# Optimization experiments

Measured on AMD Instinct MI355X. Metric: run time of the kernel, lower is better.

Reference implementation:

```python
import jax, jax.numpy as jnp
import numpy as np

NB_HEAD = 16
SIZE_PER_HEAD = 64
D_MODEL = NB_HEAD * SIZE_PER_HEAD  # 1024
B, S = 4, 2048
NEG_BIG = 1e10


def setup_inputs() -> dict:
    key = jax.random.key(0)
    ks = jax.random.split(key, 9)
    glorot = lambda k, shape: jax.random.uniform(
        k, shape, jnp.float32, -1.0, 1.0) * np.sqrt(6.0 / (shape[0] + shape[1]))
    return {
        "Q_emb": jax.random.normal(ks[0], (B, S, D_MODEL), jnp.float32),
        "K_emb": jax.random.normal(ks[1], (B, S, D_MODEL), jnp.float32),
        "V_emb": jax.random.normal(ks[2], (B, S, D_MODEL), jnp.float32),
        "Q_ini": jax.random.randint(ks[3], (B, S), 0, 50),
        "K_ini": jax.random.randint(ks[4], (B, S), 0, 50),
        "WQ": glorot(ks[5], (D_MODEL, D_MODEL)),
        "WK": glorot(ks[6], (D_MODEL, D_MODEL)),
        "WV": glorot(ks[7], (D_MODEL, D_MODEL)),
        "WO": glorot(ks[8], (D_MODEL, D_MODEL)),
    }


def _proj(x, W):
    # [B,S,D] @ [D, H*dh] -> [B,H,S,dh]
    b, s, _ = x.shape
    y = jnp.einsum('bsd,de->bse', x, W)
    return y.reshape(b, s, NB_HEAD, SIZE_PER_HEAD).transpose(0, 2, 1, 3)


def reference(Q_emb, K_emb, V_emb, Q_ini, K_ini, WQ, WK, WV, WO):
    b, sq, _ = Q_emb.shape
    sk = K_emb.shape[1]
    q = _proj(Q_emb, WQ)
    k = _proj(K_emb, WK)
    v = _proj(V_emb, WV)
    scores = jnp.einsum('bhqd,bhkd->bhqk', q, k) / jnp.sqrt(
        jnp.asarray(SIZE_PER_HEAD, scores_dtype := q.dtype))
    # pad mask: 1 where key token id != 0, broadcast over queries
    pad = (K_ini != 0).astype(scores.dtype)[:, None, None, :]  # [B,1,1,Sk]
    # sub mask: cumsum of eye along rows == lower-triangular causal mask
    causal = jnp.tril(jnp.ones((sq, sk), scores.dtype))[None, None]  # [1,1,Sq,Sk]
    mask = jnp.minimum(pad, causal)
    scores = scores - (1.0 - mask) * NEG_BIG
    attn = jax.nn.softmax(scores, axis=-1)
    ctx = jnp.einsum('bhqk,bhkd->bhqd', attn, v)
    ctx = ctx.transpose(0, 2, 1, 3).reshape(b, sq, NB_HEAD * SIZE_PER_HEAD)
    return jnp.einsum('bsd,de->bse', ctx, WO)
```

## Files before the change

### kernel.cpp

```cpp
#include <hip/hip_runtime.h>

typedef __bf16 bf16_t;
typedef __bf16 bf16x8 __attribute__((ext_vector_type(8)));
typedef float  f32x4  __attribute__((ext_vector_type(4)));

#define S_LEN 2048
#define NH    16
#define DH    64
#define DM    1024
#define BATCH 4

static __device__ __forceinline__ f32x4 mfma16(bf16x8 a, bf16x8 b, f32x4 c) {
    return __builtin_amdgcn_mfma_f32_16x16x32_bf16(a, b, c, 0, 0, 0);
}

static __device__ __forceinline__ void gl_lds16(const bf16_t* g, bf16_t* l) {
    __builtin_amdgcn_global_load_lds(
        (const __attribute__((address_space(1))) unsigned int*)g,
        (__attribute__((address_space(3))) unsigned int*)l, 16, 0, 0);
}

__global__ __launch_bounds__(256) void cvt_bf16(const float* __restrict__ s,
                                                bf16_t* __restrict__ d, int n) {
    int i = (blockIdx.x * 256 + threadIdx.x) * 8;
    if (i >= n) return;
    const float4* q = (const float4*)(s + i);
    float4 a = q[0], b = q[1];
    bf16x8 r;
    r[0] = (bf16_t)a.x; r[1] = (bf16_t)a.y; r[2] = (bf16_t)a.z; r[3] = (bf16_t)a.w;
    r[4] = (bf16_t)b.x; r[5] = (bf16_t)b.y; r[6] = (bf16_t)b.z; r[7] = (bf16_t)b.w;
    *(bf16x8*)(d + i) = r;
}

__global__ __launch_bounds__(256) void wtrans(const float* __restrict__ W,
                                              bf16_t* __restrict__ Wt, float scale) {
    __shared__ bf16_t tile[32][33];
    int x = threadIdx.x, ty = threadIdx.y;
    int bx = blockIdx.x * 32, by = blockIdx.y * 32;
#pragma unroll
    for (int i = 0; i < 4; ++i) {
        int y = ty * 4 + i;
        tile[y][x] = (bf16_t)(W[(by + y) * DM + bx + x] * scale);
    }
    __syncthreads();
#pragma unroll
    for (int i = 0; i < 4; ++i) {
        int y = ty * 4 + i;
        Wt[(bx + y) * DM + by + x] = tile[x][y];
    }
}

__global__ __launch_bounds__(256) void btrans(const bf16_t* __restrict__ src,
                                              bf16_t* __restrict__ dst,
                                              int R, int C) {
    __shared__ bf16_t tile[32][33];
    int x = threadIdx.x, ty = threadIdx.y;
    int bx = blockIdx.x * 32, by = blockIdx.y * 32;
#pragma unroll
    for (int i = 0; i < 4; ++i) {
        int y = ty * 4 + i;
        tile[y][x] = src[(size_t)(by + y) * C + bx + x];
    }
    __syncthreads();
#pragma unroll
    for (int i = 0; i < 4; ++i) {
        int y = ty * 4 + i;
        dst[(size_t)(bx + y) * R + by + x] = tile[x][y];
    }
}

template <typename CT>
__global__ __launch_bounds__(256) void gemm_nt_128(const bf16_t* __restrict__ A,
                                                   const bf16_t* __restrict__ Bt,
                                                   CT* __restrict__ C,
                                                   int M, int N, int K, float alpha) {
    __shared__ __align__(16) bf16_t As[128 * 32];
    __shared__ __align__(16) bf16_t Bs[128 * 32];
    int tid = threadIdx.x, wave = tid >> 6, lane = tid & 63;
    int l15 = lane & 15, quad = lane >> 4;
    int wm = wave >> 1, wn = wave & 1;
    int bm = blockIdx.x * 128, bn = blockIdx.y * 128;
    int lrow = lane >> 2, lk = (lane & 3) << 3;

    f32x4 acc[4][4] = {};

    for (int k0 = 0; k0 < K; k0 += 32) {
#pragma unroll
        for (int c = 0; c < 2; ++c) {
            int r = wave * 32 + c * 16 + lrow;
            gl_lds16(A  + (size_t)(bm + r) * K + k0 + lk, As + (wave * 2 + c) * 512);
            gl_lds16(Bt + (size_t)(bn + r) * K + k0 + lk, Bs + (wave * 2 + c) * 512);
        }
        __syncthreads();

        bf16x8 af[4], bfr[4];
#pragma unroll
        for (int i = 0; i < 4; ++i)
            af[i] = *(const bf16x8*)(As + (wm * 64 + i * 16 + l15) * 32 + quad * 8);
#pragma unroll
        for (int j = 0; j < 4; ++j)
            bfr[j] = *(const bf16x8*)(Bs + (wn * 64 + j * 16 + l15) * 32 + quad * 8);
#pragma unroll
        for (int i = 0; i < 4; ++i)
#pragma unroll
            for (int j = 0; j < 4; ++j)
                acc[i][j] = mfma16(af[i], bfr[j], acc[i][j]);
        __syncthreads();
    }

#pragma unroll
    for (int i = 0; i < 4; ++i)
#pragma unroll
        for (int r = 0; r < 4; ++r) {
            int row = bm + wm * 64 + i * 16 + quad * 4 + r;
#pragma unroll
            for (int j = 0; j < 4; ++j)
                C[(size_t)row * N + bn + wn * 64 + j * 16 + l15] =
                    (CT)(acc[i][j][r] * alpha);
        }
}

__global__ __launch_bounds__(256) void vmean_kernel(const bf16_t* __restrict__ Vp,
                                                    float* __restrict__ Vm) {
    __shared__ float red[4][64];
    int z = blockIdx.y;
    int c = blockIdx.x * 64 + (threadIdx.x & 63);
    int rg = threadIdx.x >> 6;
    const bf16_t* p = Vp + (size_t)z * S_LEN * DM + (size_t)rg * (S_LEN / 4) * DM + c;
    float s = 0.f;
    for (int r = 0; r < S_LEN / 4; ++r) s += (float)p[(size_t)r * DM];
    red[rg][threadIdx.x & 63] = s;
    __syncthreads();
    if (threadIdx.x < 64) {
        float t = red[0][threadIdx.x] + red[1][threadIdx.x] +
                  red[2][threadIdx.x] + red[3][threadIdx.x];
        Vm[z * DM + blockIdx.x * 64 + threadIdx.x] = t * (1.0f / S_LEN);
    }
}

__global__ __launch_bounds__(256) void attn_kernel(const bf16_t* __restrict__ Qp,
                                                   const bf16_t* __restrict__ Kp,
                                                   const bf16_t* __restrict__ VT,
                                                   const int* __restrict__ Kini,
                                                   const float* __restrict__ Vmean,
                                                   bf16_t* __restrict__ ctx,
                                                   int ldv, int nqt) {
    __shared__ __align__(16) bf16_t Ks[64 * 72];
    __shared__ __align__(16) bf16_t VsT[64 * 72];
    __shared__ __align__(16) bf16_t Ps[4][16 * 72];

    int bid = blockIdx.x;
    int qt = nqt - 1 - (bid >> 6);
    int hz = bid & 63;
    int h = hz & 15, z = hz >> 4;
    int tid = threadIdx.x, wave = tid >> 6, lane = tid & 63;
    int l15 = lane & 15, quad = lane >> 4;
    int qbase = qt * 64 + wave * 16;
    size_t rowz = (size_t)z * S_LEN;

    const bf16_t* qptr = Qp + (rowz + qbase + l15) * DM + h * DH + quad * 8;
    bf16x8 qa0 = *(const bf16x8*)qptr;
    bf16x8 qa1 = *(const bf16x8*)(qptr + 32);

    f32x4 o[4] = {};
    float m_[4], l_[4];
#pragma unroll
    for (int r = 0; r < 4; ++r) { m_[r] = -3.0e38f; l_[r] = 0.0f; }

    int srow = tid >> 2, sch = (tid & 3) << 4;
    const bf16_t* kgb = Kp + (rowz + srow) * DM + h * DH + sch;
    const bf16_t* vgb = VT + (size_t)(h * DH + srow) * ldv + rowz + sch;

    int ntiles = qt + 1;

    bf16x8 kr0 = *(const bf16x8*)kgb,        kr1 = *(const bf16x8*)(kgb + 8);
    bf16x8 vr0 = *(const bf16x8*)vgb,        vr1 = *(const bf16x8*)(vgb + 8);

    for (int kt = 0; kt < ntiles; ++kt) {
        int kb = kt * 64;
        *(bf16x8*)(Ks  + srow * 72 + sch)     = kr0;
        *(bf16x8*)(Ks  + srow * 72 + sch + 8) = kr1;
        *(bf16x8*)(VsT + srow * 72 + sch)     = vr0;
        *(bf16x8*)(VsT + srow * 72 + sch + 8) = vr1;
        __syncthreads();

        int nkb = (kt + 1 < ntiles) ? kb + 64 : kb;
        const bf16_t* kg = kgb + (size_t)nkb * DM;
        const bf16_t* vg = vgb + nkb;
        kr0 = *(const bf16x8*)kg; kr1 = *(const bf16x8*)(kg + 8);
        vr0 = *(const bf16x8*)vg; vr1 = *(const bf16x8*)(vg + 8);

        float sv[4][4];
#pragma unroll
        for (int ks = 0; ks < 4; ++ks) {
            bf16x8 kf0 = *(const bf16x8*)(Ks + (ks * 16 + l15) * 72 + quad * 8);
            bf16x8 kf1 = *(const bf16x8*)(Ks + (ks * 16 + l15) * 72 + 32 + quad * 8);
            f32x4 s = {0.f, 0.f, 0.f, 0.f};
            s = mfma16(qa0, kf0, s);
            s = mfma16(qa1, kf1, s);
            int key = kb + ks * 16 + l15;
            bool padz = (Kini[rowz + key] == 0);
#pragma unroll
            for (int r = 0; r < 4; ++r) {
                int q = qbase + quad * 4 + r;
                float val = s[r];
                if (padz || key > q) val -= 1e10f;
                sv[ks][r] = val;
            }
        }

#pragma unroll
        for (int r = 0; r < 4; ++r) {
            float mx = fmaxf(fmaxf(sv[0][r], sv[1][r]), fmaxf(sv[2][r], sv[3][r]));
#pragma unroll
            for (int d = 1; d < 16; d <<= 1) mx = fmaxf(mx, __shfl_xor(mx, d));
            float mn = fmaxf(m_[r], mx);
            float al = __expf(m_[r] - mn);
            float p0 = __expf(sv[0][r] - mn), p1 = __expf(sv[1][r] - mn);
            float p2 = __expf(sv[2][r] - mn), p3 = __expf(sv[3][r] - mn);
            float rs = (p0 + p1) + (p2 + p3);
#pragma unroll
            for (int d = 1; d < 16; d <<= 1) rs += __shfl_xor(rs, d);
            l_[r] = l_[r] * al + rs;
            m_[r] = mn;
#pragma unroll
            for (int j = 0; j < 4; ++j) o[j][r] *= al;
            int pr = (quad * 4 + r) * 72;
            Ps[wave][pr + l15]      = (bf16_t)p0;
            Ps[wave][pr + 16 + l15] = (bf16_t)p1;
            Ps[wave][pr + 32 + l15] = (bf16_t)p2;
            Ps[wave][pr + 48 + l15] = (bf16_t)p3;
        }

        bf16x8 pa0 = *(const bf16x8*)(Ps[wave] + l15 * 72 + quad * 8);
        bf16x8 pa1 = *(const bf16x8*)(Ps[wave] + l15 * 72 + 32 + quad * 8);
#pragma unroll
        for (int j = 0; j < 4; ++j) {
            bf16x8 vb0 = *(const bf16x8*)(VsT + (j * 16 + l15) * 72 + quad * 8);
            bf16x8 vb1 = *(const bf16x8*)(VsT + (j * 16 + l15) * 72 + 32 + quad * 8);
            o[j] = mfma16(pa0, vb0, o[j]);
            o[j] = mfma16(pa1, vb1, o[j]);
        }
        __syncthreads();
    }

#pragma unroll
    for (int r = 0; r < 4; ++r) {
        int q = qbase + quad * 4 + r;
        float inv = 1.0f / l_[r];
        bf16_t* cp = ctx + (rowz + q) * DM + h * DH;
        if (m_[r] < -1e9f) {
            const float* vm = Vmean + z * DM + h * DH;
#pragma unroll
            for (int j = 0; j < 4; ++j) cp[j * 16 + l15] = (bf16_t)vm[j * 16 + l15];
        } else {
#pragma unroll
            for (int j = 0; j < 4; ++j) cp[j * 16 + l15] = (bf16_t)(o[j][r] * inv);
        }
    }
}

extern "C" void kernel_launch(void* const* d_in, const int* in_sizes, int n_in,
                              void* d_out, int out_size, void* d_ws, size_t ws_size,
                              hipStream_t stream) {
    const float* Qe = (const float*)d_in[0];
    const float* Ke = (const float*)d_in[1];
    const float* Ve = (const float*)d_in[2];
    const int* Kini = (const int*)d_in[4];
    const float* WQ = (const float*)d_in[5];
    const float* WK = (const float*)d_in[6];
    const float* WV = (const float*)d_in[7];
    const float* WO = (const float*)d_in[8];
    float* out = (float*)d_out;

    const size_t EMB = (size_t)BATCH * S_LEN * DM;
    const size_t SB  = (size_t)S_LEN * DM;
    const size_t WSZ = (size_t)DM * DM;
    const size_t need_full = (6 * EMB + 4 * WSZ) * sizeof(bf16_t)
                           + (size_t)BATCH * DM * sizeof(float);

    dim3 tb32(32, 8), tg32(32, 32);

    if (ws_size >= need_full) {
        bf16_t* Qb  = (bf16_t*)d_ws;
        bf16_t* Kb  = Qb + EMB;
        bf16_t* Vb  = Kb + EMB;
        bf16_t* WQt = Vb + EMB;
        bf16_t* WKt = WQt + WSZ;
        bf16_t* WVt = WKt + WSZ;
        bf16_t* WOt = WVt + WSZ;
        bf16_t* Qp  = WOt + WSZ;
        bf16_t* Kp  = Qp + EMB;
        bf16_t* Vp  = Kp + EMB;
        float*  Vm  = (float*)(Vp + EMB);
        bf16_t* Cx  = Qp;
        bf16_t* VT  = Vb;

        int cg = (int)(EMB / (8 * 256));
        cvt_bf16<<<cg, 256, 0, stream>>>(Qe, Qb, (int)EMB);
        cvt_bf16<<<cg, 256, 0, stream>>>(Ke, Kb, (int)EMB);
        cvt_bf16<<<cg, 256, 0, stream>>>(Ve, Vb, (int)EMB);
        wtrans<<<tg32, tb32, 0, stream>>>(WQ, WQt, 0.125f);
        wtrans<<<tg32, tb32, 0, stream>>>(WK, WKt, 1.0f);
        wtrans<<<tg32, tb32, 0, stream>>>(WV, WVt, 1.0f);
        wtrans<<<tg32, tb32, 0, stream>>>(WO, WOt, 1.0f);

        dim3 gg(8192 / 128, DM / 128);
        gemm_nt_128<bf16_t><<<gg, 256, 0, stream>>>(Qb, WQt, Qp, 8192, DM, DM, 1.0f);
        gemm_nt_128<bf16_t><<<gg, 256, 0, stream>>>(Kb, WKt, Kp, 8192, DM, DM, 1.0f);
        gemm_nt_128<bf16_t><<<gg, 256, 0, stream>>>(Vb, WVt, Vp, 8192, DM, DM, 1.0f);

        btrans<<<dim3(DM / 32, 8192 / 32), tb32, 0, stream>>>(Vp, VT, 8192, DM);
        vmean_kernel<<<dim3(DM / 64, BATCH), 256, 0, stream>>>(Vp, Vm);
        attn_kernel<<<dim3((S_LEN / 64) * NH * BATCH), 256, 0, stream>>>(
            Qp, Kp, VT, Kini, Vm, Cx, 8192, S_LEN / 64);

        gemm_nt_128<float><<<gg, 256, 0, stream>>>(Cx, WOt, out, 8192, DM, DM, 1.0f);
    } else {
        bf16_t* Qb  = (bf16_t*)d_ws;
        bf16_t* Kb  = Qb + SB;
        bf16_t* Vb  = Kb + SB;
        bf16_t* WQt = Vb + SB;
        bf16_t* WKt = WQt + WSZ;
        bf16_t* WVt = WKt + WSZ;
        bf16_t* WOt = WVt + WSZ;
        bf16_t* Qp  = WOt + WSZ;
        bf16_t* Kp  = Qp + SB;
        bf16_t* Vp  = Kp + SB;
        float*  Vm  = (float*)(Vp + SB);
        bf16_t* Cx  = Qp;
        bf16_t* VT  = Vb;

        wtrans<<<tg32, tb32, 0, stream>>>(WQ, WQt, 0.125f);
        wtrans<<<tg32, tb32, 0, stream>>>(WK, WKt, 1.0f);
        wtrans<<<tg32, tb32, 0, stream>>>(WV, WVt, 1.0f);
        wtrans<<<tg32, tb32, 0, stream>>>(WO, WOt, 1.0f);

        int cg = (int)(SB / (8 * 256));
        dim3 gg(2048 / 128, DM / 128);
        for (int b = 0; b < BATCH; ++b) {
            const size_t off = (size_t)b * SB;
            cvt_bf16<<<cg, 256, 0, stream>>>(Qe + off, Qb, (int)SB);
            cvt_bf16<<<cg, 256, 0, stream>>>(Ke + off, Kb, (int)SB);
            cvt_bf16<<<cg, 256, 0, stream>>>(Ve + off, Vb, (int)SB);
            gemm_nt_128<bf16_t><<<gg, 256, 0, stream>>>(Qb, WQt, Qp, 2048, DM, DM, 1.0f);
            gemm_nt_128<bf16_t><<<gg, 256, 0, stream>>>(Kb, WKt, Kp, 2048, DM, DM, 1.0f);
            gemm_nt_128<bf16_t><<<gg, 256, 0, stream>>>(Vb, WVt, Vp, 2048, DM, DM, 1.0f);
            btrans<<<dim3(DM / 32, 2048 / 32), tb32, 0, stream>>>(Vp, VT, 2048, DM);
            vmean_kernel<<<dim3(DM / 64, 1), 256, 0, stream>>>(Vp, Vm);
            attn_kernel<<<dim3((S_LEN / 64) * NH), 256, 0, stream>>>(
                Qp, Kp, VT, Kini + (size_t)b * S_LEN, Vm, Cx, 2048, S_LEN / 64);
            gemm_nt_128<float><<<gg, 256, 0, stream>>>(Cx, WOt, out + off, 2048, DM, DM, 1.0f);
        }
    }
}
```

Baseline: 427.8 us.

## Transpose attention MFMA layout, precompute pad bias, lazy rescale, causal mask only on diagonal

Swaps the MFMA operand order so each lane owns one query row, which lets softmax max/sum reductions use two cross-quad shuffles instead of four-step butterflies per row. The pad mask becomes an additive bf16 bias precomputed in LDS once per block, and the causal mask is applied only on the diagonal tile. Online-softmax rescaling is skipped unless some row max grows by more than 8. Output is staged through LDS and written with 16-byte vector stores. This trades extra LDS and a preamble pass over Kini for less per-tile ALU and shuffle work, and it relies on the threshold bound to keep the exponentials from overflowing.

```diff
diff --git a/kernel.cpp b/kernel.cpp
--- a/kernel.cpp
+++ b/kernel.cpp
@@ -2,6 +2,7 @@
 
 typedef __bf16 bf16_t;
 typedef __bf16 bf16x8 __attribute__((ext_vector_type(8)));
+typedef __bf16 bf16x4 __attribute__((ext_vector_type(4)));
 typedef float  f32x4  __attribute__((ext_vector_type(4)));
 
 #define S_LEN 2048
@@ -12,6 +13,13 @@
 
 static __device__ __forceinline__ f32x4 mfma16(bf16x8 a, bf16x8 b, f32x4 c) {
     return __builtin_amdgcn_mfma_f32_16x16x32_bf16(a, b, c, 0, 0, 0);
+}
+
+static __device__ __forceinline__ f32x4 fmax4(f32x4 a, f32x4 b) {
+    f32x4 r;
+    r[0] = fmaxf(a[0], b[0]); r[1] = fmaxf(a[1], b[1]);
+    r[2] = fmaxf(a[2], b[2]); r[3] = fmaxf(a[3], b[3]);
+    return r;
 }
 
 static __device__ __forceinline__ void gl_lds16(const bf16_t* g, bf16_t* l) {
@@ -148,6 +156,7 @@
     __shared__ __align__(16) bf16_t Ks[64 * 72];
     __shared__ __align__(16) bf16_t VsT[64 * 72];
     __shared__ __align__(16) bf16_t Ps[4][16 * 72];
+    __shared__ bf16_t padb[2048];
 
     int bid = blockIdx.x;
     int qt = nqt - 1 - (bid >> 6);
@@ -157,21 +166,23 @@
     int l15 = lane & 15, quad = lane >> 4;
     int qbase = qt * 64 + wave * 16;
     size_t rowz = (size_t)z * S_LEN;
+    int ntiles = qt + 1;
+    int nkeys = ntiles * 64;
+
+    for (int i = tid; i < nkeys; i += 256)
+        padb[i] = (Kini[rowz + i] == 0) ? (bf16_t)(-1e10f) : (bf16_t)(0.0f);
 
     const bf16_t* qptr = Qp + (rowz + qbase + l15) * DM + h * DH + quad * 8;
     bf16x8 qa0 = *(const bf16x8*)qptr;
     bf16x8 qa1 = *(const bf16x8*)(qptr + 32);
 
     f32x4 o[4] = {};
-    float m_[4], l_[4];
-#pragma unroll
-    for (int r = 0; r < 4; ++r) { m_[r] = -3.0e38f; l_[r] = 0.0f; }
+    float m_ = -3.0e38f, l_ = 0.0f;
+    int q = qbase + l15;
 
     int srow = tid >> 2, sch = (tid & 3) << 4;
     const bf16_t* kgb = Kp + (rowz + srow) * DM + h * DH + sch;
     const bf16_t* vgb = VT + (size_t)(h * DH + srow) * ldv + rowz + sch;
-
-    int ntiles = qt + 1;
 
     bf16x8 kr0 = *(const bf16x8*)kgb,        kr1 = *(const bf16x8*)(kgb + 8);
     bf16x8 vr0 = *(const bf16x8*)vgb,        vr1 = *(const bf16x8*)(vgb + 8);
@@ -190,46 +201,58 @@
         kr0 = *(const bf16x8*)kg; kr1 = *(const bf16x8*)(kg + 8);
         vr0 = *(const bf16x8*)vg; vr1 = *(const bf16x8*)(vg + 8);
 
-        float sv[4][4];
+        f32x4 sv[4];
 #pragma unroll
         for (int ks = 0; ks < 4; ++ks) {
             bf16x8 kf0 = *(const bf16x8*)(Ks + (ks * 16 + l15) * 72 + quad * 8);
             bf16x8 kf1 = *(const bf16x8*)(Ks + (ks * 16 + l15) * 72 + 32 + quad * 8);
             f32x4 s = {0.f, 0.f, 0.f, 0.f};
-            s = mfma16(qa0, kf0, s);
-            s = mfma16(qa1, kf1, s);
-            int key = kb + ks * 16 + l15;
-            bool padz = (Kini[rowz + key] == 0);
-#pragma unroll
-            for (int r = 0; r < 4; ++r) {
-                int q = qbase + quad * 4 + r;
-                float val = s[r];
-                if (padz || key > q) val -= 1e10f;
-                sv[ks][r] = val;
-            }
-        }
-
-#pragma unroll
-        for (int r = 0; r < 4; ++r) {
-            float mx = fmaxf(fmaxf(sv[0][r], sv[1][r]), fmaxf(sv[2][r], sv[3][r]));
-#pragma unroll
-            for (int d = 1; d < 16; d <<= 1) mx = fmaxf(mx, __shfl_xor(mx, d));
-            float mn = fmaxf(m_[r], mx);
-            float al = __expf(m_[r] - mn);
-            float p0 = __expf(sv[0][r] - mn), p1 = __expf(sv[1][r] - mn);
-            float p2 = __expf(sv[2][r] - mn), p3 = __expf(sv[3][r] - mn);
-            float rs = (p0 + p1) + (p2 + p3);
-#pragma unroll
-            for (int d = 1; d < 16; d <<= 1) rs += __shfl_xor(rs, d);
-            l_[r] = l_[r] * al + rs;
-            m_[r] = mn;
-#pragma unroll
-            for (int j = 0; j < 4; ++j) o[j][r] *= al;
-            int pr = (quad * 4 + r) * 72;
-            Ps[wave][pr + l15]      = (bf16_t)p0;
-            Ps[wave][pr + 16 + l15] = (bf16_t)p1;
-            Ps[wave][pr + 32 + l15] = (bf16_t)p2;
-            Ps[wave][pr + 48 + l15] = (bf16_t)p3;
+            s = mfma16(kf0, qa0, s);
+            s = mfma16(kf1, qa1, s);
+            bf16x4 pb = *(const bf16x4*)(padb + kb + ks * 16 + quad * 4);
+#pragma unroll
+            for (int r = 0; r < 4; ++r) s[r] += (float)pb[r];
+            sv[ks] = s;
+        }
+        if (kt == ntiles - 1) {
+#pragma unroll
+            for (int ks = 0; ks < 4; ++ks)
+#pragma unroll
+                for (int r = 0; r < 4; ++r)
+                    if (kb + ks * 16 + quad * 4 + r > q) sv[ks][r] = -1e10f;
+        }
+
+        f32x4 m4 = fmax4(fmax4(sv[0], sv[1]), fmax4(sv[2], sv[3]));
+        float mx = fmaxf(fmaxf(m4[0], m4[1]), fmaxf(m4[2], m4[3]));
+        mx = fmaxf(mx, __shfl_xor(mx, 16));
+        mx = fmaxf(mx, __shfl_xor(mx, 32));
+
+        if (__any(mx > m_ + 8.0f)) {
+            float mn = fmaxf(m_, mx);
+            float al = __expf(m_ - mn);
+#pragma unroll
+            for (int j = 0; j < 4; ++j) o[j] *= al;
+            l_ *= al; m_ = mn;
+        }
+
+#pragma unroll
+        for (int ks = 0; ks < 4; ++ks) {
+            f32x4 s = sv[ks];
+#pragma unroll
+            for (int r = 0; r < 4; ++r) s[r] = __expf(s[r] - m_);
+            sv[ks] = s;
+        }
+        f32x4 t4 = (sv[0] + sv[1]) + (sv[2] + sv[3]);
+        float rs = (t4[0] + t4[1]) + (t4[2] + t4[3]);
+        rs += __shfl_xor(rs, 16);
+        rs += __shfl_xor(rs, 32);
+        l_ += rs;
+#pragma unroll
+        for (int ks = 0; ks < 4; ++ks) {
+            bf16x4 pk;
+#pragma unroll
+            for (int r = 0; r < 4; ++r) pk[r] = (bf16_t)sv[ks][r];
+            *(bf16x4*)(Ps[wave] + l15 * 72 + ks * 16 + quad * 4) = pk;
         }
 
         bf16x8 pa0 = *(const bf16x8*)(Ps[wave] + l15 * 72 + quad * 8);
@@ -238,26 +261,42 @@
         for (int j = 0; j < 4; ++j) {
             bf16x8 vb0 = *(const bf16x8*)(VsT + (j * 16 + l15) * 72 + quad * 8);
             bf16x8 vb1 = *(const bf16x8*)(VsT + (j * 16 + l15) * 72 + 32 + quad * 8);
-            o[j] = mfma16(pa0, vb0, o[j]);
-            o[j] = mfma16(pa1, vb1, o[j]);
+            o[j] = mfma16(vb0, pa0, o[j]);
+            o[j] = mfma16(vb1, pa1, o[j]);
         }
         __syncthreads();
     }
 
-#pragma unroll
-    for (int r = 0; r < 4; ++r) {
-        int q = qbase + quad * 4 + r;
-        float inv = 1.0f / l_[r];
-        bf16_t* cp = ctx + (rowz + q) * DM + h * DH;
-        if (m_[r] < -1e9f) {
-            const float* vm = Vmean + z * DM + h * DH;
-#pragma unroll
-            for (int j = 0; j < 4; ++j) cp[j * 16 + l15] = (bf16_t)vm[j * 16 + l15];
-        } else {
-#pragma unroll
-            for (int j = 0; j < 4; ++j) cp[j * 16 + l15] = (bf16_t)(o[j][r] * inv);
-        }
-    }
+    float inv = 1.0f / l_;
+    bool dead = (m_ < -1e9f);
+    if (__any(dead)) {
+        const float* vm = Vmean + z * DM + h * DH;
+#pragma unroll
+        for (int j = 0; j < 4; ++j) {
+            bf16x4 c;
+#pragma unroll
+            for (int r = 0; r < 4; ++r) {
+                int dh = j * 16 + quad * 4 + r;
+                float val = dead ? vm[dh] : o[j][r] * inv;
+                c[r] = (bf16_t)val;
+            }
+            *(bf16x4*)(Ps[wave] + l15 * 72 + j * 16 + quad * 4) = c;
+        }
+    } else {
+#pragma unroll
+        for (int j = 0; j < 4; ++j) {
+            bf16x4 c;
+#pragma unroll
+            for (int r = 0; r < 4; ++r) c[r] = (bf16_t)(o[j][r] * inv);
+            *(bf16x4*)(Ps[wave] + l15 * 72 + j * 16 + quad * 4) = c;
+        }
+    }
+    int rr = lane >> 2, cc = (lane & 3) * 16;
+    bf16x8 t0 = *(const bf16x8*)(Ps[wave] + rr * 72 + cc);
+    bf16x8 t1 = *(const bf16x8*)(Ps[wave] + rr * 72 + cc + 8);
+    bf16_t* cp = ctx + (rowz + qbase + rr) * DM + h * DH + cc;
+    *(bf16x8*)cp = t0;
+    *(bf16x8*)(cp + 8) = t1;
 }
 
 extern "C" void kernel_launch(void* const* d_in, const int* in_sizes, int n_in,
```

After: 383.2 us. -10.4%, faster.
